# Performance work log

Hardware: AMD Instinct MI355X
Metric: run time of the kernel (lower is better)

Reference implementation:

```python
import jax, jax.numpy as jnp
import numpy as np

FEATURE_DIM = 6272
UNITS = 32
B, L = 8, 256

def setup_inputs() -> dict:
    key = jax.random.key(0)
    k1, k2, k3, k4, k5 = jax.random.split(key, 5)
    return {
        "inputs": jax.random.normal(k1, (B, L, FEATURE_DIM), dtype=jnp.float32),
        "Wt": jax.random.normal(k2, (FEATURE_DIM, UNITS), dtype=jnp.float32) * 0.02,
        "bh": jax.random.normal(k3, (UNITS,), dtype=jnp.float32),
        "Wa": jax.random.normal(k4, (UNITS, 1), dtype=jnp.float32) * 0.02,
        "ba": jax.random.normal(k5, (1,), dtype=jnp.float32),
    }

def reference(inputs, Wt, bh, Wa, ba):
    # q == k: both projected through Wt (original code reuses Wt for both)
    p = jnp.einsum('blf,fu->blu', inputs, Wt)            # [B, L, U]
    # additive (Bahdanau-style) pairwise combine: [B, L, L, U]
    beta = jnp.tanh(p[:, :, None, :] + p[:, None, :, :] + bh)
    alpha = jnp.einsum('bqku,uo->bqk', beta, Wa) + ba[0]  # [B, L, L]
    alpha = jax.nn.sigmoid(alpha)
    a = jax.nn.softmax(alpha, axis=-1)                    # softmax over keys
    c_r = jnp.einsum('bqk,bkf->bqf', a, inputs)           # [B, L, F]
    return c_r
```

## Files before the change

kernel.cpp:

```cpp
#include <hip/hip_runtime.h>
#include <hip/hip_bf16.h>
#include <math.h>

#define FDIM 6272
#define LQ   256
#define BN   8
#define UDIM 32
#define BL   (BN*LQ)

typedef short  short8 __attribute__((ext_vector_type(8)));
typedef float  f32x4  __attribute__((ext_vector_type(4)));

static __device__ __forceinline__ ushort f2bf(float f) {
    __hip_bfloat16 h = __float2bfloat16(f);
    return *(ushort*)&h;
}
static __device__ __forceinline__ float fexp2(float x) {
    float r;
    asm volatile("v_exp_f32 %0, %1 \n s_nop 1" : "=v"(r) : "v"(x));
    return r;
}
static __device__ __forceinline__ float frcp(float x) {
    float r;
    asm volatile("v_rcp_f32 %0, %1 \n s_nop 1" : "=v"(r) : "v"(x));
    return r;
}
static __device__ __forceinline__ float tanh_fast(float v) {
    return 1.f - 2.f * frcp(1.f + fexp2(v * 2.88539008177793f));
}

__global__ __launch_bounds__(256)
void k_wtt(const float* __restrict__ Wt, ushort* __restrict__ wtt,
           float* __restrict__ pb) {
    const int gid = blockIdx.x * 256 + threadIdx.x;
    const int u = gid / 784, fg = gid % 784;
    ushort v[8];
    #pragma unroll
    for (int j = 0; j < 8; ++j)
        v[j] = f2bf(Wt[(size_t)(8 * fg + j) * UDIM + u]);
    *(uint4*)(wtt + (size_t)u * FDIM + 8 * fg) = *(uint4*)v;

    if (gid < BL * UDIM / 4)
        ((float4*)pb)[gid] = make_float4(0.f, 0.f, 0.f, 0.f);
}

__global__ __launch_bounds__(256)
void k1_mfma(const float* __restrict__ x, const ushort* __restrict__ wtt,
             float* __restrict__ pb, ushort* __restrict__ xb16) {
    const int t    = threadIdx.x;
    const int wv   = t >> 6, lane = t & 63;
    const int n16  = lane & 15, quad = lane >> 4;
    const int row0 = blockIdx.x * 32 + 16 * (wv & 1);
    const int u0   = 16 * (wv >> 1);
    const int f0   = blockIdx.y * 896;

    const float*  xr = x    + (size_t)(row0 + n16) * FDIM + f0 + quad * 8;
    const ushort* wr = wtt  + (size_t)(u0   + n16) * FDIM + f0 + quad * 8;
    ushort*       xw = xb16 + (size_t)(row0 + n16) * FDIM + f0 + quad * 8;

    f32x4 acc = (f32x4){0.f, 0.f, 0.f, 0.f};

    #pragma unroll 4
    for (int c = 0; c < 28; ++c) {
        const float4 a0 = *(const float4*)(xr + c * 32);
        const float4 a1 = *(const float4*)(xr + c * 32 + 4);
        short8 af;
        af[0] = (short)f2bf(a0.x); af[1] = (short)f2bf(a0.y);
        af[2] = (short)f2bf(a0.z); af[3] = (short)f2bf(a0.w);
        af[4] = (short)f2bf(a1.x); af[5] = (short)f2bf(a1.y);
        af[6] = (short)f2bf(a1.z); af[7] = (short)f2bf(a1.w);
        if (wv < 2)
            *(short8*)(xw + c * 32) = af;
        const short8 bf = *(const short8*)(wr + c * 32);
        acc = __builtin_amdgcn_mfma_f32_16x16x32_bf16(af, bf, acc, 0, 0, 0);
    }

    #pragma unroll
    for (int r = 0; r < 4; ++r)
        atomicAdd(&pb[(size_t)(row0 + quad * 4 + r) * UDIM + u0 + n16], acc[r]);
}

__global__ __launch_bounds__(256)
void k2_attn(const float* __restrict__ pb, const float* __restrict__ bh,
             const float* __restrict__ Wa, const float* __restrict__ ba,
             ushort* __restrict__ ab) {
    const int bq = blockIdx.x;
    const int b  = bq >> 8, q = bq & 255;
    const int k  = threadIdx.x;

    __shared__ float pk_s[LQ * 33];
    __shared__ float pq_s[UDIM];
    __shared__ float wa_s[UDIM];
    __shared__ float red[4];

    if (k < UDIM) wa_s[k] = Wa[k];
    const float* pbb = pb + (size_t)b * LQ * UDIM;
    #pragma unroll
    for (int i = 0; i < 32; ++i) {
        int idx = k + i * 256;
        pk_s[(idx >> 5) * 33 + (idx & 31)] = pbb[idx];
    }
    __syncthreads();
    if (k < UDIM) pq_s[k] = pk_s[q * 33 + k] + bh[k];
    __syncthreads();

    const float* pk = &pk_s[k * 33];
    float s = 0.f;
    #pragma unroll
    for (int u = 0; u < UDIM; ++u)
        s = fmaf(tanh_fast(pq_s[u] + pk[u]), wa_s[u], s);

    const float alpha = frcp(1.f + fexp2(-(s + ba[0]) * 1.44269504088896f));
    const float e = fexp2(alpha * 1.44269504088896f);

    float v = e;
    #pragma unroll
    for (int m = 1; m < 64; m <<= 1) v += __shfl_xor(v, m, 64);
    if ((k & 63) == 0) red[k >> 6] = v;
    __syncthreads();
    const float tot = red[0] + red[1] + red[2] + red[3];

    ab[(size_t)bq * LQ + k] = f2bf(e * frcp(tot));
}

__global__ __launch_bounds__(256)
void k3_fused(const ushort* __restrict__ xb16, const ushort* __restrict__ ab,
              float* __restrict__ out) {
    __shared__ ushort Bs[2][64 * 72];

    const int t    = threadIdx.x;
    const int f0   = blockIdx.x * 64;
    const int b    = blockIdx.y;
    const int wv   = t >> 6;
    const int lane = t & 63;
    const int n16  = lane & 15;
    const int quad = lane >> 4;
    const int g    = t >> 4;
    const int kp   = t & 15;

    const ushort* xb  = xb16 + (size_t)b * LQ * FDIM + f0 + 4 * g;
    const ushort* abb = ab   + (size_t)b * LQ * LQ;

    f32x4 acc[4][4];
    #pragma unroll
    for (int mf = 0; mf < 4; ++mf)
        #pragma unroll
        for (int nf = 0; nf < 4; ++nf)
            acc[mf][nf] = (f32x4){0.f, 0.f, 0.f, 0.f};

    uint2 r0, r1, r2, r3;
#define LDX(kc) do {                                                      \
        r0 = *(const uint2*)(xb + (size_t)((kc) + 2 * kp     ) * FDIM);   \
        r1 = *(const uint2*)(xb + (size_t)((kc) + 2 * kp +  1) * FDIM);   \
        r2 = *(const uint2*)(xb + (size_t)((kc) + 2 * kp + 32) * FDIM);   \
        r3 = *(const uint2*)(xb + (size_t)((kc) + 2 * kp + 33) * FDIM);   \
    } while (0)
#define STX(bufi) do {                                                    \
        unsigned* bw = (unsigned*)(Bs[bufi]);                             \
        bw[(4 * g + 0) * 36 + kp]      = (r0.x & 0xffffu) | (r1.x << 16); \
        bw[(4 * g + 1) * 36 + kp]      = (r0.x >> 16) | (r1.x & 0xffff0000u); \
        bw[(4 * g + 2) * 36 + kp]      = (r0.y & 0xffffu) | (r1.y << 16); \
        bw[(4 * g + 3) * 36 + kp]      = (r0.y >> 16) | (r1.y & 0xffff0000u); \
        bw[(4 * g + 0) * 36 + kp + 16] = (r2.x & 0xffffu) | (r3.x << 16); \
        bw[(4 * g + 1) * 36 + kp + 16] = (r2.x >> 16) | (r3.x & 0xffff0000u); \
        bw[(4 * g + 2) * 36 + kp + 16] = (r2.y & 0xffffu) | (r3.y << 16); \
        bw[(4 * g + 3) * 36 + kp + 16] = (r2.y >> 16) | (r3.y & 0xffff0000u); \
    } while (0)

    LDX(0);
    STX(0);

    for (int c = 0; c < 4; ++c) {
        if (c < 3) LDX((c + 1) * 64);
        short8 af[4][2];
        #pragma unroll
        for (int mf = 0; mf < 4; ++mf)
            #pragma unroll
            for (int h = 0; h < 2; ++h)
                af[mf][h] = *(const short8*)(abb
                    + (size_t)(64 * wv + 16 * mf + n16) * LQ
                    + c * 64 + h * 32 + quad * 8);
        __syncthreads();
        const ushort* bsc = Bs[c & 1];
        #pragma unroll
        for (int h = 0; h < 2; ++h)
            #pragma unroll
            for (int nf = 0; nf < 4; ++nf) {
                const short8 bf = *(const short8*)(bsc + (16 * nf + n16) * 72
                                                   + h * 32 + quad * 8);
                #pragma unroll
                for (int mf = 0; mf < 4; ++mf)
                    acc[mf][nf] = __builtin_amdgcn_mfma_f32_16x16x32_bf16(
                        af[mf][h], bf, acc[mf][nf], 0, 0, 0);
            }
        if (c < 3) STX((c + 1) & 1);
    }
#undef LDX
#undef STX

    float* ob = out + ((size_t)b * LQ + 64 * wv + quad * 4) * FDIM + f0 + n16;
    #pragma unroll
    for (int mf = 0; mf < 4; ++mf)
        #pragma unroll
        for (int nf = 0; nf < 4; ++nf)
            #pragma unroll
            for (int r = 0; r < 4; ++r)
                ob[(size_t)(16 * mf + r) * FDIM + 16 * nf] = acc[mf][nf][r];
}

extern "C" void kernel_launch(void* const* d_in, const int* in_sizes, int n_in,
                              void* d_out, int out_size, void* d_ws, size_t ws_size,
                              hipStream_t stream) {
    const float* x  = (const float*)d_in[0];
    const float* Wt = (const float*)d_in[1];
    const float* bh = (const float*)d_in[2];
    const float* Wa = (const float*)d_in[3];
    const float* ba = (const float*)d_in[4];
    float* out = (float*)d_out;

    float*  pb   = (float*)d_ws;
    ushort* ab   = (ushort*)((char*)d_ws + 262144);
    ushort* wtt  = (ushort*)((char*)d_ws + 262144 + 1048576);
    ushort* xb16 = (ushort*)((char*)d_ws + 262144 + 1048576 + 524288);

    k_wtt<<<98, 256, 0, stream>>>(Wt, wtt, pb);
    k1_mfma<<<dim3(64, 7), 256, 0, stream>>>(x, wtt, pb, xb16);
    k2_attn<<<BL, 256, 0, stream>>>(pb, bh, Wa, ba, ab);
    k3_fused<<<dim3(98, 8), 256, 0, stream>>>(xb16, ab, out);
}
```

Measured before the change: 162.2 us.

## Fuse weight transpose into projection, replace atomics with partial sums, batch queries

The separate Wt transpose/convert kernel is removed. Each projection block now converts its own 896-feature slice of Wt to bf16 in shared memory. Atomic accumulation of the projection is replaced by per-split partial buffers that the attention kernel sums on load. The attention kernel also handles 4 queries per block instead of 1, which spreads the per-batch pk staging over more work. Together these drop a launch, the zeroing pass and atomic contention, at the cost of redundant Wt conversion per block and extra partial-buffer reads.

```diff
diff --git a/kernel.cpp b/kernel.cpp
--- a/kernel.cpp
+++ b/kernel.cpp
@@ -7,6 +7,7 @@
 #define BN   8
 #define UDIM 32
 #define BL   (BN*LQ)
+#define WTS  904
 
 typedef short  short8 __attribute__((ext_vector_type(8)));
 typedef float  f32x4  __attribute__((ext_vector_type(4)));
@@ -30,32 +31,35 @@
 }
 
 __global__ __launch_bounds__(256)
-void k_wtt(const float* __restrict__ Wt, ushort* __restrict__ wtt,
-           float* __restrict__ pb) {
-    const int gid = blockIdx.x * 256 + threadIdx.x;
-    const int u = gid / 784, fg = gid % 784;
-    ushort v[8];
-    #pragma unroll
-    for (int j = 0; j < 8; ++j)
-        v[j] = f2bf(Wt[(size_t)(8 * fg + j) * UDIM + u]);
-    *(uint4*)(wtt + (size_t)u * FDIM + 8 * fg) = *(uint4*)v;
-
-    if (gid < BL * UDIM / 4)
-        ((float4*)pb)[gid] = make_float4(0.f, 0.f, 0.f, 0.f);
-}
-
-__global__ __launch_bounds__(256)
-void k1_mfma(const float* __restrict__ x, const ushort* __restrict__ wtt,
-             float* __restrict__ pb, ushort* __restrict__ xb16) {
-    const int t    = threadIdx.x;
+void k1_mfma(const float* __restrict__ x, const float* __restrict__ Wt,
+             float* __restrict__ pbp, ushort* __restrict__ xb16) {
+    __shared__ ushort wtt_s[UDIM * WTS];
+
+    const int t  = threadIdx.x;
+    const int f0 = blockIdx.y * 896;
+
+    {
+        const int fl0 = t >> 3;
+        const int u4  = (t & 7) * 4;
+        #pragma unroll
+        for (int s = 0; s < 28; ++s) {
+            const int fl = s * 32 + fl0;
+            const float4 w4 = *(const float4*)(Wt + (size_t)(f0 + fl) * UDIM + u4);
+            wtt_s[(u4 + 0) * WTS + fl] = f2bf(w4.x);
+            wtt_s[(u4 + 1) * WTS + fl] = f2bf(w4.y);
+            wtt_s[(u4 + 2) * WTS + fl] = f2bf(w4.z);
+            wtt_s[(u4 + 3) * WTS + fl] = f2bf(w4.w);
+        }
+    }
+    __syncthreads();
+
     const int wv   = t >> 6, lane = t & 63;
     const int n16  = lane & 15, quad = lane >> 4;
     const int row0 = blockIdx.x * 32 + 16 * (wv & 1);
     const int u0   = 16 * (wv >> 1);
-    const int f0   = blockIdx.y * 896;
-
-    const float*  xr = x    + (size_t)(row0 + n16) * FDIM + f0 + quad * 8;
-    const ushort* wr = wtt  + (size_t)(u0   + n16) * FDIM + f0 + quad * 8;
+
+    const float*  xr = x + (size_t)(row0 + n16) * FDIM + f0 + quad * 8;
+    const ushort* wr = wtt_s + (u0 + n16) * WTS + quad * 8;
     ushort*       xw = xb16 + (size_t)(row0 + n16) * FDIM + f0 + quad * 8;
 
     f32x4 acc = (f32x4){0.f, 0.f, 0.f, 0.f};
@@ -75,52 +79,75 @@
         acc = __builtin_amdgcn_mfma_f32_16x16x32_bf16(af, bf, acc, 0, 0, 0);
     }
 
+    float* pb = pbp + (size_t)blockIdx.y * BL * UDIM;
     #pragma unroll
     for (int r = 0; r < 4; ++r)
-        atomicAdd(&pb[(size_t)(row0 + quad * 4 + r) * UDIM + u0 + n16], acc[r]);
+        pb[(size_t)(row0 + quad * 4 + r) * UDIM + u0 + n16] = acc[r];
 }
 
 __global__ __launch_bounds__(256)
-void k2_attn(const float* __restrict__ pb, const float* __restrict__ bh,
+void k2_attn(const float* __restrict__ pbp, const float* __restrict__ bh,
              const float* __restrict__ Wa, const float* __restrict__ ba,
              ushort* __restrict__ ab) {
-    const int bq = blockIdx.x;
-    const int b  = bq >> 8, q = bq & 255;
-    const int k  = threadIdx.x;
+    const int blk = blockIdx.x;
+    const int b   = blk >> 6, qt = blk & 63;
+    const int k   = threadIdx.x;
 
     __shared__ float pk_s[LQ * 33];
-    __shared__ float pq_s[UDIM];
+    __shared__ float pq_s[4][UDIM];
     __shared__ float wa_s[UDIM];
-    __shared__ float red[4];
+    __shared__ float red[4][4];
 
     if (k < UDIM) wa_s[k] = Wa[k];
-    const float* pbb = pb + (size_t)b * LQ * UDIM;
-    #pragma unroll
-    for (int i = 0; i < 32; ++i) {
-        int idx = k + i * 256;
-        pk_s[(idx >> 5) * 33 + (idx & 31)] = pbb[idx];
-    }
-    __syncthreads();
-    if (k < UDIM) pq_s[k] = pk_s[q * 33 + k] + bh[k];
+    const float* pbb = pbp + (size_t)b * LQ * UDIM;
+    #pragma unroll
+    for (int i = 0; i < 8; ++i) {
+        const int e = 4 * k + 1024 * i;
+        float4 v = *(const float4*)(pbb + e);
+        #pragma unroll
+        for (int y = 1; y < 7; ++y) {
+            const float4 p = *(const float4*)(pbb + (size_t)y * BL * UDIM + e);
+            v.x += p.x; v.y += p.y; v.z += p.z; v.w += p.w;
+        }
+        float* d = &pk_s[(e >> 5) * 33 + (e & 31)];
+        d[0] = v.x; d[1] = v.y; d[2] = v.z; d[3] = v.w;
+    }
+    __syncthreads();
+    if (k < 4 * UDIM) {
+        const int j = k >> 5, u = k & 31;
+        pq_s[j][u] = pk_s[(qt * 4 + j) * 33 + u] + bh[u];
+    }
     __syncthreads();
 
     const float* pk = &pk_s[k * 33];
-    float s = 0.f;
-    #pragma unroll
-    for (int u = 0; u < UDIM; ++u)
-        s = fmaf(tanh_fast(pq_s[u] + pk[u]), wa_s[u], s);
-
-    const float alpha = frcp(1.f + fexp2(-(s + ba[0]) * 1.44269504088896f));
-    const float e = fexp2(alpha * 1.44269504088896f);
-
-    float v = e;
-    #pragma unroll
-    for (int m = 1; m < 64; m <<= 1) v += __shfl_xor(v, m, 64);
-    if ((k & 63) == 0) red[k >> 6] = v;
-    __syncthreads();
-    const float tot = red[0] + red[1] + red[2] + red[3];
-
-    ab[(size_t)bq * LQ + k] = f2bf(e * frcp(tot));
+    float pkr[UDIM];
+    #pragma unroll
+    for (int u = 0; u < UDIM; ++u) pkr[u] = pk[u];
+
+    const float ba0 = ba[0];
+    float e4[4];
+    #pragma unroll
+    for (int j = 0; j < 4; ++j) {
+        float s = 0.f;
+        #pragma unroll
+        for (int u = 0; u < UDIM; ++u)
+            s = fmaf(tanh_fast(pq_s[j][u] + pkr[u]), wa_s[u], s);
+
+        const float alpha = frcp(1.f + fexp2(-(s + ba0) * 1.44269504088896f));
+        const float e = fexp2(alpha * 1.44269504088896f);
+        e4[j] = e;
+
+        float v = e;
+        #pragma unroll
+        for (int m = 1; m < 64; m <<= 1) v += __shfl_xor(v, m, 64);
+        if ((k & 63) == 0) red[j][k >> 6] = v;
+    }
+    __syncthreads();
+    #pragma unroll
+    for (int j = 0; j < 4; ++j) {
+        const float tot = red[j][0] + red[j][1] + red[j][2] + red[j][3];
+        ab[((size_t)b * LQ + qt * 4 + j) * LQ + k] = f2bf(e4[j] * frcp(tot));
+    }
 }
 
 __global__ __launch_bounds__(256)
@@ -218,13 +245,11 @@
     const float* ba = (const float*)d_in[4];
     float* out = (float*)d_out;
 
-    float*  pb   = (float*)d_ws;
-    ushort* ab   = (ushort*)((char*)d_ws + 262144);
-    ushort* wtt  = (ushort*)((char*)d_ws + 262144 + 1048576);
-    ushort* xb16 = (ushort*)((char*)d_ws + 262144 + 1048576 + 524288);
-
-    k_wtt<<<98, 256, 0, stream>>>(Wt, wtt, pb);
-    k1_mfma<<<dim3(64, 7), 256, 0, stream>>>(x, wtt, pb, xb16);
-    k2_attn<<<BL, 256, 0, stream>>>(pb, bh, Wa, ba, ab);
+    float*  pbp  = (float*)d_ws;
+    ushort* ab   = (ushort*)((char*)d_ws + 2097152);
+    ushort* xb16 = (ushort*)((char*)d_ws + 2097152 + 1048576);
+
+    k1_mfma<<<dim3(64, 7), 256, 0, stream>>>(x, Wt, pbp, xb16);
+    k2_attn<<<512, 256, 0, stream>>>(pbp, bh, Wa, ba, ab);
     k3_fused<<<dim3(98, 8), 256, 0, stream>>>(xb16, ab, out);
 }
```

Measured after the change: 161.2 us. Within noise of the previous version (-0.6%).
